# Kernel tuning notes

Hardware: AMD Instinct MI355X
Metric: run time of the kernel (lower is better)

Reference implementation:

```python
import jax, jax.numpy as jnp
import numpy as np

N, E, IN, H, T = 100000, 1600000, 10, 64, 10


def setup_inputs() -> dict:
    key = jax.random.key(0)
    ks = jax.random.split(key, 24)
    w = lambda k, shape, s=0.05: jax.random.normal(k, shape, jnp.float32) * s
    return {
        "x": w(ks[0], (N, IN), 1.0),
        "edge_attr": w(ks[1], (E, T), 1.0),
        "gcn1_w": w(ks[2], (IN, H)), "gcn1_b": jnp.zeros((H,), jnp.float32),
        "e_w1": w(ks[3], (3 * T, H)), "e_b1": jnp.zeros((H,), jnp.float32),
        "e_w2": w(ks[4], (H, H)), "e_b2": jnp.zeros((H,), jnp.float32),
        "gcn2_w": w(ks[5], (2 * H, H)), "gcn2_b": jnp.zeros((H,), jnp.float32),
        "gcn3_w": w(ks[6], (H, IN)), "gcn3_b": jnp.zeros((IN,), jnp.float32),
        "l1_w": w(ks[7], (2 * IN, IN)), "l1_b": jnp.zeros((IN,), jnp.float32),
        "l2_w": w(ks[8], (IN, 128)), "l2_b": jnp.zeros((128,), jnp.float32),
        "l3_w": w(ks[9], (128, 32)), "l3_b": jnp.zeros((32,), jnp.float32),
        "l4_w": w(ks[10], (32, 2)), "l4_b": jnp.zeros((2,), jnp.float32),
        "edge_index": jax.random.randint(ks[11], (2, E), 0, N),
    }


def reference(x, edge_attr, gcn1_w, gcn1_b, e_w1, e_b1, e_w2, e_b2,
              gcn2_w, gcn2_b, gcn3_w, gcn3_b, l1_w, l1_b, l2_w, l2_b,
              l3_w, l3_b, l4_w, l4_b, edge_index):
    src, dst = edge_index[0], edge_index[1]  # j -> i (message flows src->dst)
    # GCN symmetric norm with self loops: deg counted on target, +1 self loop
    deg = 1.0 + jax.ops.segment_sum(jnp.ones((E,), jnp.float32), dst, num_segments=N)
    dis = deg ** -0.5  # [N]
    edge_norm = (dis[src] * dis[dst])[:, None]  # [E,1]

    def gcn(h, w, b):
        hw = h @ w  # [N,out]
        agg = jax.ops.segment_sum(hw[src] * edge_norm, dst, num_segments=N)
        agg = agg + hw * (dis * dis)[:, None]  # self-loop term, norm = 1/deg
        return agg + b

    out1 = jax.nn.relu(gcn(x, gcn1_w, gcn1_b))
    # EdgeConv: gather x_i (dst), x_j (src), concat edge_attr, MLP, scatter-max
    m = jnp.concatenate([x[dst], x[src], edge_attr], axis=1)  # [E, 3T]
    m = jax.nn.relu(m @ e_w1 + e_b1) @ e_w2 + e_b2  # [E, H]
    agg = jax.ops.segment_max(m, dst, num_segments=N)
    agg = jnp.where(jnp.isfinite(agg), agg, 0.0)  # isolated nodes -> 0
    oute = jax.nn.relu(agg)

    out2 = jax.nn.relu(gcn(jnp.concatenate([out1, oute], axis=1), gcn2_w, gcn2_b))
    out3 = jax.nn.relu(gcn(out2, gcn3_w, gcn3_b))
    h = jnp.concatenate([x, out3], axis=1)  # [N, 2*IN]
    h = jax.nn.softplus(h @ l1_w + l1_b)
    h = jax.nn.softplus(h @ l2_w + l2_b)
    h = jax.nn.softplus(h @ l3_w + l3_b)
    h = h @ l4_w + l4_b  # [N, 2]
    return (h[:, 0], h[:, 1])
```

## Files before the change

### kernel.cpp

```cpp
#include <hip/hip_runtime.h>
#include <hip/hip_bf16.h>

typedef unsigned int u32;
typedef unsigned short u16;
typedef _Float16 f16;
typedef _Float16 f16x8 __attribute__((ext_vector_type(8)));
typedef float f32x4 __attribute__((ext_vector_type(4)));
typedef u32 u32x4 __attribute__((ext_vector_type(4)));

#define DEV static __device__ __forceinline__

#define O_G1   0
#define O_G1b  640
#define O_W1   704
#define O_B1   2624
#define O_W2   2688
#define O_B2   6784
#define O_G2   6848
#define O_G2b  15040
#define O_G3   15104
#define O_G3b  15744
#define O_L1   15754
#define O_L1b  15954
#define O_L2t  15964
#define O_L2b  17244
#define O_L3   17372
#define O_L3b  21468
#define O_L4t  21500
#define O_L4b  21564
#define O_WF1  21568
#define O_WF2  22592
#define WTOT   24640

#define ECNB   32

DEV float bfu(u16 h){ return __uint_as_float(((u32)h) << 16); }
DEV float bflo(u32 u){ return __uint_as_float(u << 16); }
DEV float bfhi(u32 u){ return __uint_as_float(u & 0xffff0000u); }
DEV u16 f2bf(float x){
  __hip_bfloat16 b = __float2bfloat16(x);
  return *(u16*)&b;
}
DEV float rdf(const void* p, int idx, int isf32){
  return isf32 ? ((const float*)p)[idx] : bfu(((const u16*)p)[idx]);
}
DEV void load10_bf(const u32* __restrict__ p, float* f){
  u32 a0=p[0],a1=p[1],a2=p[2],a3=p[3],a4=p[4];
  f[0]=bflo(a0); f[1]=bfhi(a0);
  f[2]=bflo(a1); f[3]=bfhi(a1);
  f[4]=bflo(a2); f[5]=bfhi(a2);
  f[6]=bflo(a3); f[7]=bfhi(a3);
  f[8]=bflo(a4); f[9]=bfhi(a4);
}
DEV void load10_any(const void* base, size_t row, int isf32, float* f){
  if (isf32){
    const float* p = (const float*)base + row*10;
    #pragma unroll
    for (int k=0;k<10;k++) f[k] = p[k];
  } else {
    load10_bf((const u32*)base + row*5, f);
  }
}
DEV float softplusf(float x){ return fmaxf(x,0.f) + log1pf(__expf(-fabsf(x))); }

DEV int permk(int k){
  if (k < 8)  return k;
  if (k < 16) return 10 + (k-8);
  if (k < 24) return 20 + (k-16);
  if (k == 24) return 8;
  if (k == 25) return 9;
  if (k == 26) return 18;
  if (k == 27) return 19;
  if (k == 28) return 28;
  if (k == 29) return 29;
  return -1;
}
DEV u32 packh2(float a, float b){
  union { f16 h[2]; u32 u; } t;
  t.h[0] = (f16)a; t.h[1] = (f16)b;
  return t.u;
}

__global__ __launch_bounds__(256) void k_detect(
    const u32* p0, const u32* p1, const u32* p2, const u32* p3,
    const u32* p4, const u32* p5, const u32* p6, const u32* p7,
    const u32* p8, const u32* p9, const u32* p10,const u32* p11,
    const u32* p12,const u32* p13,const u32* p14,const u32* p15,
    const u32* p16,const u32* p17,const u32* p18,const u32* p19,
    int* __restrict__ flags, int N_, int E_)
{
  int a = blockIdx.x;
  const u32* p;
  int elems;
  switch (a){
    case 0:  p=p0;  elems=N_*10; break;
    case 1:  p=p1;  elems=E_*10; break;
    case 2:  p=p2;  elems=640;  break;
    case 3:  p=p3;  elems=64;   break;
    case 4:  p=p4;  elems=1920; break;
    case 5:  p=p5;  elems=64;   break;
    case 6:  p=p6;  elems=4096; break;
    case 7:  p=p7;  elems=64;   break;
    case 8:  p=p8;  elems=8192; break;
    case 9:  p=p9;  elems=64;   break;
    case 10: p=p10; elems=640;  break;
    case 11: p=p11; elems=10;   break;
    case 12: p=p12; elems=200;  break;
    case 13: p=p13; elems=10;   break;
    case 14: p=p14; elems=1280; break;
    case 15: p=p15; elems=128;  break;
    case 16: p=p16; elems=4096; break;
    case 17: p=p17; elems=32;   break;
    case 18: p=p18; elems=64;   break;
    default: p=p19; elems=2;    break;
  }
  int nw = elems/2; if (nw > 512) nw = 512; if (nw < 1) nw = 1;
  int localA = 0, localZ = 0;
  for (int i=threadIdx.x; i<nw; i+=256){
    u32 w = p[i];
    u32 ex = (w >> 7) & 0xffu;
    if (ex >= 0x90u) localA++;
    if ((w & 0xffffu) == 0u) localZ++;
  }
  int packed = (localA << 16) | localZ;
  __shared__ int red[4];
  #pragma unroll
  for (int off=32; off; off>>=1) packed += __shfl_down(packed, off);
  if ((threadIdx.x & 63) == 0) red[threadIdx.x>>6] = packed;
  __syncthreads();
  if (threadIdx.x == 0){
    int s = red[0]+red[1]+red[2]+red[3];
    int sA = s >> 16, sZ = s & 0xffff;
    flags[a] = (sA * 16 >= nw || sZ * 4 >= nw * 3) ? 1 : 0;
  }
}

__global__ __launch_bounds__(256) void k_prep(
    const void* g1w, const void* g1b, const void* ew1, const void* eb1,
    const void* ew2, const void* eb2, const void* g2w, const void* g2b,
    const void* g3w, const void* g3b, const void* l1w, const void* l1b,
    const void* l2w, const void* l2b, const void* l3w, const void* l3b,
    const void* l4w, const void* l4b,
    const int* __restrict__ flags, float* __restrict__ W)
{
  int t = threadIdx.x;
  int f2=flags[2],f3=flags[3],f4=flags[4],f5=flags[5],f6=flags[6],f7=flags[7];
  int f8=flags[8],f9=flags[9],f10=flags[10],f11=flags[11],f12=flags[12],f13=flags[13];
  int f14=flags[14],f15=flags[15],f16=flags[16],f17=flags[17],f18=flags[18],f19=flags[19];
  for (int i=t;i<640;i+=256)  W[O_G1+i]  = rdf(g1w,i,f2);
  for (int i=t;i<64;i+=256)   W[O_G1b+i] = rdf(g1b,i,f3);
  for (int i=t;i<1920;i+=256) W[O_W1+i]  = rdf(ew1,i,f4);
  for (int i=t;i<64;i+=256)   W[O_B1+i]  = rdf(eb1,i,f5);
  for (int i=t;i<4096;i+=256) W[O_W2+i]  = rdf(ew2,i,f6);
  for (int i=t;i<64;i+=256)   W[O_B2+i]  = rdf(eb2,i,f7);
  for (int i=t;i<8192;i+=256) W[O_G2+i]  = rdf(g2w,i,f8);
  for (int i=t;i<64;i+=256)   W[O_G2b+i] = rdf(g2b,i,f9);
  for (int i=t;i<640;i+=256)  W[O_G3+i]  = rdf(g3w,i,f10);
  for (int i=t;i<10;i+=256)   W[O_G3b+i] = rdf(g3b,i,f11);
  for (int i=t;i<200;i+=256)  W[O_L1+i]  = rdf(l1w,i,f12);
  for (int i=t;i<10;i+=256)   W[O_L1b+i] = rdf(l1b,i,f13);
  for (int i=t;i<1280;i+=256){ int o=i/10,k=i-o*10; W[O_L2t+i]=rdf(l2w,k*128+o,f14); }
  for (int i=t;i<128;i+=256)  W[O_L2b+i] = rdf(l2b,i,f15);
  for (int i=t;i<4096;i+=256) W[O_L3+i]  = rdf(l3w,i,f16);
  for (int i=t;i<32;i+=256)   W[O_L3b+i] = rdf(l3b,i,f17);
  for (int i=t;i<64;i+=256){ int c=i>>5,j=i&31; W[O_L4t+i]=rdf(l4w,j*2+c,f18); }
  for (int i=t;i<2;i+=256)    W[O_L4b+i] = rdf(l4b,i,f19);
  u32* Wu = (u32*)W;
  for (int i=t;i<1024;i+=256){
    int l=i&63, q=(i>>6)&3, c=i>>8;
    int k0=(l>>4)*8+2*q, col=c*16+(l&15);
    int r0=permk(k0), r1=permk(k0+1);
    float v0 = (r0<0)?0.f:rdf(ew1,r0*64+col,f4);
    float v1 = (r1<0)?0.f:rdf(ew1,r1*64+col,f4);
    Wu[O_WF1+i] = packh2(v0,v1);
  }
  for (int i=t;i<2048;i+=256){
    int l=i&63, q=(i>>6)&3, h2=(i>>8)&1, c=i>>9;
    int k0=32*h2+(l>>4)*8+2*q, col=c*16+(l&15);
    Wu[O_WF2+i] = packh2(rdf(ew2,k0*64+col,f6), rdf(ew2,(k0+1)*64+col,f6));
  }
}

__global__ __launch_bounds__(256) void k_init(int* __restrict__ cnt, int N_)
{
  int i = blockIdx.x*256 + threadIdx.x;
  if (i < N_) cnt[i] = 0;
}

__global__ __launch_bounds__(256) void k_count(const int* __restrict__ ei, int* __restrict__ cnt, int E_)
{
  int e = blockIdx.x*256 + threadIdx.x;
  if (e >= E_) return;
  atomicAdd(&cnt[ei[E_+e]], 1);
}

__global__ __launch_bounds__(1024) void k_bsum(const int* __restrict__ cnt, int* __restrict__ bsum, int N_)
{
  int i = blockIdx.x*1024 + threadIdx.x;
  int v = (i < N_) ? cnt[i] : 0;
  #pragma unroll
  for (int off=32; off; off>>=1) v += __shfl_down(v, off);
  __shared__ int ws_[16];
  if ((threadIdx.x & 63) == 0) ws_[threadIdx.x>>6] = v;
  __syncthreads();
  if (threadIdx.x == 0){
    int s = 0;
    #pragma unroll
    for (int j=0;j<16;j++) s += ws_[j];
    bsum[blockIdx.x] = s;
  }
}

__global__ __launch_bounds__(128) void k_scan_small(const int* __restrict__ bsum, int* __restrict__ boff, int NB)
{
  int t = threadIdx.x;
  int v = (t < NB) ? bsum[t] : 0;
  int lane = t & 63, w = t >> 6;
  int x = v;
  #pragma unroll
  for (int off=1; off<64; off<<=1){ int y=__shfl_up(x,off); if (lane>=off) x+=y; }
  __shared__ int t2[2];
  if (lane==63) t2[w]=x;
  __syncthreads();
  if (w==1) x += t2[0];
  boff[t] = x - v;
}

__global__ __launch_bounds__(1024) void k_scan_final(
    int* __restrict__ cnt, const int* __restrict__ boff,
    int* __restrict__ rp, float* __restrict__ dis, int N_, int E_)
{
  int i = blockIdx.x*1024 + threadIdx.x;
  int v = (i < N_) ? cnt[i] : 0;
  int lane = threadIdx.x & 63, w = threadIdx.x >> 6;
  int x = v;
  #pragma unroll
  for (int off=1; off<64; off<<=1){ int y=__shfl_up(x,off); if (lane>=off) x+=y; }
  __shared__ int wp[16];
  if (lane==63) wp[w]=x;
  __syncthreads();
  if (threadIdx.x==0){
    int run=0;
    #pragma unroll
    for (int j=0;j<16;j++){ int t=wp[j]; wp[j]=run; run+=t; }
  }
  __syncthreads();
  int incl = x + wp[w] + boff[blockIdx.x];
  if (i < N_){
    rp[i]  = incl - v;
    dis[i] = rsqrtf(1.f + (float)v);
    cnt[i] = 0;
  }
  if (i == 0) rp[N_] = E_;
}

__global__ __launch_bounds__(256) void k_fill(
    const int* __restrict__ ei, const int* __restrict__ rp, int* __restrict__ cnt,
    int4* __restrict__ csr, int E_)
{
  int e = blockIdx.x*256 + threadIdx.x;
  if (e >= E_) return;
  int s = ei[e], d = ei[E_+e];
  int pos = rp[d] + atomicAdd(&cnt[d], 1);
  csr[pos] = make_int4(s, e, d, 0);
}

#define EC_EMIT \
  if (run >= 0){ int bb = run*64 + x; \
    atomicMax(&nodemax[bb],    __float_as_int(e0)); \
    atomicMax(&nodemax[bb+16], __float_as_int(e1)); \
    atomicMax(&nodemax[bb+32], __float_as_int(e2)); \
    atomicMax(&nodemax[bb+48], __float_as_int(e3)); }
#define EC_STEP(DD, RR) { \
  float t0=fmaxf(mcv[0][RR],0.f), t1=fmaxf(mcv[1][RR],0.f), \
        t2=fmaxf(mcv[2][RR],0.f), t3=fmaxf(mcv[3][RR],0.f); \
  if (DD == run){ e0=fmaxf(e0,t0); e1=fmaxf(e1,t1); e2=fmaxf(e2,t2); e3=fmaxf(e3,t3); } \
  else { EC_EMIT; run = DD; e0=t0; e1=t1; e2=t2; e3=t3; } }

__global__ __launch_bounds__(256) void k_edgeconv(
    const void* __restrict__ xv, const void* __restrict__ eav,
    const int* __restrict__ rp, const int4* __restrict__ csr,
    const float* __restrict__ W, const int* __restrict__ flags,
    float* __restrict__ oute, int N_, int E_)
{
  __shared__ int nodemax[ECNB*64];
  __shared__ u32 hbuf[4][16*36];
  int tid = threadIdx.x;
  int l = tid & 63, wv = tid >> 6;
  int x = l & 15, g = l >> 4;
  int n0 = blockIdx.x * ECNB;
  if (n0 >= N_) return;
  int nend = n0 + ECNB; if (nend > N_) nend = N_;
  #pragma unroll
  for (int i=0;i<ECNB/4;i++) nodemax[i*256 + tid] = 0;
  int fx = flags[0], fea = flags[1];
  const u32* Wu = (const u32*)W;
  union FU { u32 u[4]; f16x8 v; };
  union HU { f16 h[8]; u32 u[4]; f16x8 v; };
  FU w1u[4];
  #pragma unroll
  for (int c=0;c<4;c++){
    #pragma unroll
    for (int q=0;q<4;q++) w1u[c].u[q] = Wu[O_WF1 + (c*4+q)*64 + l];
  }
  FU w2u[4][2];
  #pragma unroll
  for (int c=0;c<4;c++){
    #pragma unroll
    for (int h=0;h<2;h++){
      #pragma unroll
      for (int q=0;q<4;q++) w2u[c][h].u[q] = Wu[O_WF2 + ((c*2+h)*4+q)*64 + l];
    }
  }
  float b1v[4], b2v[4];
  #pragma unroll
  for (int c=0;c<4;c++){ b1v[c] = (W+O_B1)[c*16 + x]; b2v[c] = (W+O_B2)[c*16 + x]; }
  int pbase = rp[n0], pend = rp[nend];
  int ntiles = (pend - pbase + 15) >> 4;
  u32* hb = hbuf[wv];
  __syncthreads();

  for (int t = wv; t < ntiles; t += 4){
    int p0 = pbase + t*16;
    int eA = p0 + x; if (eA > E_-1) eA = E_-1;
    int4 ce = csr[eA];
    HU af;
    u32 exv = 0;
    if (g < 3){
      long row; const void* base; int isf;
      if (g==0){ row = ce.z; base = xv;  isf = fx; }
      else if (g==1){ row = ce.x; base = xv;  isf = fx; }
      else { row = ce.y; base = eav; isf = fea; }
      if (isf){
        const float* p = (const float*)base + row*10;
        #pragma unroll
        for (int j=0;j<8;j++) af.h[j] = (f16)p[j];
        exv = packh2(p[8], p[9]);
      } else {
        const u32* p = (const u32*)base + row*5;
        u32 a0=p[0],a1=p[1],a2=p[2],a3=p[3],a4=p[4];
        af.h[0]=(f16)bflo(a0); af.h[1]=(f16)bfhi(a0);
        af.h[2]=(f16)bflo(a1); af.h[3]=(f16)bfhi(a1);
        af.h[4]=(f16)bflo(a2); af.h[5]=(f16)bfhi(a2);
        af.h[6]=(f16)bflo(a3); af.h[7]=(f16)bfhi(a3);
        exv = packh2(bflo(a4), bfhi(a4));
      }
    }
    u32 ge0 = (u32)__shfl((int)exv, x);
    u32 ge1 = (u32)__shfl((int)exv, x+16);
    u32 ge2 = (u32)__shfl((int)exv, x+32);
    if (g == 3){ af.u[0]=ge0; af.u[1]=ge1; af.u[2]=ge2; af.u[3]=0; }
    int pe = p0 + 4*g;
    int dz = ce.z;
    int d0 = __shfl(dz, 4*g+0); d0 = (pe   < pend) ? d0 - n0 : -1;
    int d1 = __shfl(dz, 4*g+1); d1 = (pe+1 < pend) ? d1 - n0 : -1;
    int d2 = __shfl(dz, 4*g+2); d2 = (pe+2 < pend) ? d2 - n0 : -1;
    int d3 = __shfl(dz, 4*g+3); d3 = (pe+3 < pend) ? d3 - n0 : -1;
    f32x4 z = {0.f,0.f,0.f,0.f};
    f32x4 hc[4];
    #pragma unroll
    for (int c=0;c<4;c++)
      hc[c] = __builtin_amdgcn_mfma_f32_16x16x32_f16(af.v, w1u[c].v, z, 0, 0, 0);
    #pragma unroll
    for (int r=0;r<4;r++){
      u32 pk0,pk1,pk2,pk3;
      {
        float hv = fmaxf(hc[0][r] + b1v[0], 0.f);
        union { f16 h; u16 u; } cv; cv.h=(f16)hv; u32 mine=cv.u;
        u32 other=(u32)__shfl_xor((int)mine,1,64);
        pk0 = (x&1) ? (other|(mine<<16)) : (mine|(other<<16));
      }{
        float hv = fmaxf(hc[1][r] + b1v[1], 0.f);
        union { f16 h; u16 u; } cv; cv.h=(f16)hv; u32 mine=cv.u;
        u32 other=(u32)__shfl_xor((int)mine,1,64);
        pk1 = (x&1) ? (other|(mine<<16)) : (mine|(other<<16));
      }{
        float hv = fmaxf(hc[2][r] + b1v[2], 0.f);
        union { f16 h; u16 u; } cv; cv.h=(f16)hv; u32 mine=cv.u;
        u32 other=(u32)__shfl_xor((int)mine,1,64);
        pk2 = (x&1) ? (other|(mine<<16)) : (mine|(other<<16));
      }{
        float hv = fmaxf(hc[3][r] + b1v[3], 0.f);
        union { f16 h; u16 u; } cv; cv.h=(f16)hv; u32 mine=cv.u;
        u32 other=(u32)__shfl_xor((int)mine,1,64);
        pk3 = (x&1) ? (other|(mine<<16)) : (mine|(other<<16));
      }
      int edge = 4*g + r;
      int par = (x&1) ? 16 : 0;
      hb[edge*36 + par + (x>>1)]     = (x&1) ? pk2 : pk0;
      hb[edge*36 + 8 + par + (x>>1)] = (x&1) ? pk3 : pk1;
    }
    asm volatile("s_waitcnt lgkmcnt(0)" ::: "memory");
    HU a2f[2];
    #pragma unroll
    for (int h=0;h<2;h++){
      const u32x4* p = (const u32x4*)&hb[x*36 + g*4 + 16*h];
      u32x4 tv = *p;
      a2f[h].u[0]=tv[0]; a2f[h].u[1]=tv[1]; a2f[h].u[2]=tv[2]; a2f[h].u[3]=tv[3];
    }
    f32x4 mcv[4];
    #pragma unroll
    for (int c=0;c<4;c++){
      f32x4 bi = {b2v[c],b2v[c],b2v[c],b2v[c]};
      f32x4 acc = __builtin_amdgcn_mfma_f32_16x16x32_f16(a2f[0].v, w2u[c][0].v, bi, 0, 0, 0);
      mcv[c]    = __builtin_amdgcn_mfma_f32_16x16x32_f16(a2f[1].v, w2u[c][1].v, acc, 0, 0, 0);
    }
    int run = -2; float e0=0.f,e1=0.f,e2=0.f,e3=0.f;
    EC_STEP(d0,0) EC_STEP(d1,1) EC_STEP(d2,2) EC_STEP(d3,3)
    EC_EMIT;
  }
  __syncthreads();
  int tot = (nend - n0) * 64;
  for (int i = tid; i < tot; i += 256)
    oute[(size_t)n0*64 + i] = __int_as_float(nodemax[i]);
}

__global__ __launch_bounds__(256) void k_aggx(
    const void* __restrict__ xv, const int* __restrict__ rp,
    const int4* __restrict__ csr, const float* __restrict__ dis,
    const int* __restrict__ flags, float* __restrict__ sx, int N_)
{
  int i = blockIdx.x*256 + threadIdx.x;
  if (i >= N_) return;
  int fx = flags[0];
  float di = dis[i], d2 = di*di;
  float acc[10], ac2[10], tA[10], tB[10], tC[10], tD[10];
  load10_any(xv, (size_t)i, fx, tA);
  #pragma unroll
  for (int f=0;f<10;f++){ acc[f] = tA[f]*d2; ac2[f] = 0.f; }
  int b = rp[i], en = rp[i+1];
  int p = b;
  for (; p+3 < en; p += 4){
    int s0 = csr[p].x, s1 = csr[p+1].x, s2 = csr[p+2].x, s3 = csr[p+3].x;
    float m0 = dis[s0]*di, m1 = dis[s1]*di, m2 = dis[s2]*di, m3 = dis[s3]*di;
    load10_any(xv, (size_t)s0, fx, tA);
    load10_any(xv, (size_t)s1, fx, tB);
    load10_any(xv, (size_t)s2, fx, tC);
    load10_any(xv, (size_t)s3, fx, tD);
    #pragma unroll
    for (int f=0;f<10;f++){
      acc[f] = fmaf(tA[f], m0, acc[f]);
      ac2[f] = fmaf(tB[f], m1, ac2[f]);
      acc[f] = fmaf(tC[f], m2, acc[f]);
      ac2[f] = fmaf(tD[f], m3, ac2[f]);
    }
  }
  for (; p < en; p++){
    int s0 = csr[p].x; float m0 = dis[s0]*di;
    load10_any(xv, (size_t)s0, fx, tA);
    #pragma unroll
    for (int f=0;f<10;f++) acc[f] = fmaf(tA[f], m0, acc[f]);
  }
  float* o = sx + (size_t)i*10;
  #pragma unroll
  for (int f=0;f<10;f++) o[f] = acc[f] + ac2[f];
}

__global__ __launch_bounds__(256) void k_hw2(
    const float* __restrict__ sx, const float* __restrict__ oute,
    const float* __restrict__ W, u16* __restrict__ hw2o, int N_)
{
  int i = blockIdx.x*256 + threadIdx.x;
  if (i >= N_) return;
  float sv[10];
  const float* srow = sx + (size_t)i*10;
  #pragma unroll
  for (int f=0;f<10;f++) sv[f] = srow[f];
  const float* __restrict__ G1  = W + O_G1;
  const float* __restrict__ G1b = W + O_G1b;
  const float* __restrict__ G2  = W + O_G2;
  float hw[64];
  #pragma unroll
  for (int f=0;f<64;f++) hw[f] = 0.f;
  #pragma unroll 1
  for (int k=0;k<64;k++){
    float o1 = G1b[k];
    #pragma unroll
    for (int j=0;j<10;j++) o1 = fmaf(sv[j], G1[j*64+k], o1);
    o1 = fmaxf(o1, 0.f);
    const float* __restrict__ wt = G2 + k*64;
    #pragma unroll
    for (int f=0;f<64;f++) hw[f] = fmaf(o1, wt[f], hw[f]);
  }
  const float* orow = oute + (size_t)i*64;
  #pragma unroll 1
  for (int k=0;k<64;k++){
    float ov = orow[k];
    const float* __restrict__ wb = G2 + (64+k)*64;
    #pragma unroll
    for (int f=0;f<64;f++) hw[f] = fmaf(ov, wb[f], hw[f]);
  }
  u16* out = hw2o + (size_t)i*64;
  #pragma unroll
  for (int f=0;f<64;f++) out[f] = f2bf(hw[f]);
}

__global__ __launch_bounds__(256) void k_agg64(
    const u16* __restrict__ hw2, const int* __restrict__ rp,
    const int4* __restrict__ csr, const float* __restrict__ dis,
    const float* __restrict__ W, float* __restrict__ out2, int N_)
{
  int i = (blockIdx.x*256 + threadIdx.x) >> 6;
  int lane = threadIdx.x & 63;
  if (i >= N_) return;
  int e4 = lane >> 4, c4 = lane & 15;
  float di = dis[i];
  int b = rp[i], en = rp[i+1];
  const uint2* __restrict__ h2 = (const uint2*)hw2;
  float a0=0.f,a1=0.f,a2=0.f,a3=0.f;
  float b0=0.f,b1=0.f,b2=0.f,b3=0.f;
  int p = b + e4;
  int sA = (p   < en) ? csr[p].x   : 0;
  int sB = (p+4 < en) ? csr[p+4].x : 0;
  for (; p + 4 < en; p += 8){
    int sAn = (p+8  < en) ? csr[p+8].x  : 0;
    int sBn = (p+12 < en) ? csr[p+12].x : 0;
    float nmA = dis[sA]*di, nmB = dis[sB]*di;
    uint2 wA = h2[(size_t)sA*16 + c4];
    uint2 wB = h2[(size_t)sB*16 + c4];
    a0 = fmaf(bflo(wA.x), nmA, a0); a1 = fmaf(bfhi(wA.x), nmA, a1);
    a2 = fmaf(bflo(wA.y), nmA, a2); a3 = fmaf(bfhi(wA.y), nmA, a3);
    b0 = fmaf(bflo(wB.x), nmB, b0); b1 = fmaf(bfhi(wB.x), nmB, b1);
    b2 = fmaf(bflo(wB.y), nmB, b2); b3 = fmaf(bfhi(wB.y), nmB, b3);
    sA = sAn; sB = sBn;
  }
  if (p < en){
    float nmA = dis[sA]*di;
    uint2 wA = h2[(size_t)sA*16 + c4];
    a0 = fmaf(bflo(wA.x), nmA, a0); a1 = fmaf(bfhi(wA.x), nmA, a1);
    a2 = fmaf(bflo(wA.y), nmA, a2); a3 = fmaf(bfhi(wA.y), nmA, a3);
  }
  a0 += b0; a1 += b1; a2 += b2; a3 += b3;
  a0 += __shfl_xor(a0,16); a1 += __shfl_xor(a1,16);
  a2 += __shfl_xor(a2,16); a3 += __shfl_xor(a3,16);
  a0 += __shfl_xor(a0,32); a1 += __shfl_xor(a1,32);
  a2 += __shfl_xor(a2,32); a3 += __shfl_xor(a3,32);
  if (e4 == 0){
    uint2 ws2 = h2[(size_t)i*16 + c4];
    float d2 = di*di;
    const float* G2b = W + O_G2b;
    float4 o;
    o.x = fmaxf(fmaf(bflo(ws2.x), d2, a0) + G2b[4*c4],   0.f);
    o.y = fmaxf(fmaf(bfhi(ws2.x), d2, a1) + G2b[4*c4+1], 0.f);
    o.z = fmaxf(fmaf(bflo(ws2.y), d2, a2) + G2b[4*c4+2], 0.f);
    o.w = fmaxf(fmaf(bfhi(ws2.y), d2, a3) + G2b[4*c4+3], 0.f);
    *(float4*)(out2 + (size_t)i*64 + 4*c4) = o;
  }
}

__global__ __launch_bounds__(256) void k_hw3(
    const float* __restrict__ out2, const float* __restrict__ W,
    float* __restrict__ hw3, int N_)
{
  int i = blockIdx.x*256 + threadIdx.x;
  if (i >= N_) return;
  const float* row = out2 + (size_t)i*64;
  const float* __restrict__ G3 = W + O_G3;
  float a[10];
  #pragma unroll
  for (int f=0;f<10;f++) a[f] = 0.f;
  #pragma unroll 1
  for (int k=0;k<64;k++){
    float v = row[k];
    const float* __restrict__ w = G3 + k*10;
    #pragma unroll
    for (int f=0;f<10;f++) a[f] = fmaf(v, w[f], a[f]);
  }
  float* o = hw3 + (size_t)i*10;
  #pragma unroll
  for (int f=0;f<10;f++) o[f] = a[f];
}

__global__ __launch_bounds__(256) void k_final(
    const void* __restrict__ xv, const float* __restrict__ hw3,
    const int* __restrict__ rp, const int4* __restrict__ csr,
    const float* __restrict__ dis, const int* __restrict__ flags,
    const float* __restrict__ W, float* __restrict__ out, int N_)
{
  int i = blockIdx.x*256 + threadIdx.x;
  if (i >= N_) return;
  int fx = flags[0];
  float di = dis[i];
  float a[10], a2v[10];
  const float* hrow = hw3 + (size_t)i*10;
  #pragma unroll
  for (int f=0;f<10;f++){ a[f] = hrow[f]*di*di; a2v[f] = 0.f; }
  int b = rp[i], en = rp[i+1];
  int p = b;
  for (; p+3 < en; p += 4){
    int s0 = csr[p].x, s1 = csr[p+1].x, s2 = csr[p+2].x, s3 = csr[p+3].x;
    float m0 = dis[s0]*di, m1 = dis[s1]*di, m2 = dis[s2]*di, m3 = dis[s3]*di;
    const float* r0p = hw3 + (size_t)s0*10;
    const float* r1p = hw3 + (size_t)s1*10;
    const float* r2p = hw3 + (size_t)s2*10;
    const float* r3p = hw3 + (size_t)s3*10;
    #pragma unroll
    for (int f=0;f<10;f++){
      a[f]   = fmaf(r0p[f], m0, a[f]);
      a2v[f] = fmaf(r1p[f], m1, a2v[f]);
      a[f]   = fmaf(r2p[f], m2, a[f]);
      a2v[f] = fmaf(r3p[f], m3, a2v[f]);
    }
  }
  for (; p < en; p++){
    int s0 = csr[p].x; float m0 = dis[s0]*di;
    const float* r0p = hw3 + (size_t)s0*10;
    #pragma unroll
    for (int f=0;f<10;f++) a[f] = fmaf(r0p[f], m0, a[f]);
  }
  #pragma unroll
  for (int f=0;f<10;f++) a[f] += a2v[f];
  const float* G3b = W + O_G3b;
  float h20[20];
  load10_any(xv, (size_t)i, fx, h20);
  #pragma unroll
  for (int f=0;f<10;f++) h20[10+f] = fmaxf(a[f] + G3b[f], 0.f);
  const float* __restrict__ L1  = W + O_L1;
  const float* __restrict__ L1b = W + O_L1b;
  float h1[10];
  #pragma unroll
  for (int f=0;f<10;f++) h1[f] = L1b[f];
  #pragma unroll
  for (int k=0;k<20;k++){
    float v = h20[k];
    const float* __restrict__ w = L1 + k*10;
    #pragma unroll
    for (int f=0;f<10;f++) h1[f] = fmaf(v, w[f], h1[f]);
  }
  #pragma unroll
  for (int f=0;f<10;f++) h1[f] = softplusf(h1[f]);
  const float* __restrict__ L2t = W + O_L2t;
  const float* __restrict__ L2b = W + O_L2b;
  const float* __restrict__ L3  = W + O_L3;
  const float* __restrict__ L3b = W + O_L3b;
  float h3a[32];
  #pragma unroll
  for (int j=0;j<32;j++) h3a[j] = L3b[j];
  #pragma unroll 1
  for (int o=0;o<128;o++){
    float s2 = L2b[o];
    const float* __restrict__ wt = L2t + o*10;
    #pragma unroll
    for (int k=0;k<10;k++) s2 = fmaf(h1[k], wt[k], s2);
    s2 = softplusf(s2);
    const float* __restrict__ w3 = L3 + o*32;
    #pragma unroll
    for (int j=0;j<32;j++) h3a[j] = fmaf(s2, w3[j], h3a[j]);
  }
  const float* L4t = W + O_L4t;
  const float* L4b = W + O_L4b;
  float r0 = L4b[0], r1 = L4b[1];
  #pragma unroll
  for (int j=0;j<32;j++){
    float h3 = softplusf(h3a[j]);
    r0 = fmaf(h3, L4t[j],    r0);
    r1 = fmaf(h3, L4t[32+j], r1);
  }
  out[i]      = r0;
  out[N_ + i] = r1;
}

extern "C" void kernel_launch(void* const* d_in, const int* in_sizes, int n_in,
                              void* d_out, int out_size, void* d_ws, size_t ws_size,
                              hipStream_t stream)
{
  const void* xv  = d_in[0];
  const void* eav = d_in[1];
  const int*  ei  = (const int*)d_in[20];
  int N_ = in_sizes[0] / 10;
  int E_ = in_sizes[1] / 10;

  float* W = (float*)d_ws;
  size_t off = WTOT;
  int*   cnt   = (int*)(W + off);   off += (size_t)N_;
  int*   rp    = (int*)(W + off);   off += (size_t)N_ + 1;
  float* dis   = (float*)(W + off); off += (size_t)N_;
  int*   bsum  = (int*)(W + off);   off += 256;
  int*   boff  = (int*)(W + off);   off += 256;
  int*   flags = (int*)(W + off);   off += 32;
  off = (off + 3) & ~(size_t)3;
  int4*  csr   = (int4*)(W + off);  off += (size_t)E_ * 4;
  float* oute  = (float*)(W + off);
  float* out2  = oute;
  off += (size_t)N_ * 64;
  u16*   hw2   = (u16*)(W + off);   off += (size_t)N_ * 32;
  float* sx    = (float*)(W + off);
  float* hw3   = sx;
  off += (size_t)N_ * 10;

  if (ws_size < off * sizeof(float)) return;

  int gN = (N_ + 255)/256, gE = (E_ + 255)/256;
  int NB = (N_ + 1023)/1024;

  k_detect<<<20,256,0,stream>>>(
      (const u32*)d_in[0],(const u32*)d_in[1],
      (const u32*)d_in[2],(const u32*)d_in[3],(const u32*)d_in[4],(const u32*)d_in[5],
      (const u32*)d_in[6],(const u32*)d_in[7],(const u32*)d_in[8],(const u32*)d_in[9],
      (const u32*)d_in[10],(const u32*)d_in[11],(const u32*)d_in[12],(const u32*)d_in[13],
      (const u32*)d_in[14],(const u32*)d_in[15],(const u32*)d_in[16],(const u32*)d_in[17],
      (const u32*)d_in[18],(const u32*)d_in[19],
      flags, N_, E_);
  k_prep<<<1,256,0,stream>>>(
      d_in[2],d_in[3],d_in[4],d_in[5],d_in[6],d_in[7],d_in[8],d_in[9],
      d_in[10],d_in[11],d_in[12],d_in[13],d_in[14],d_in[15],d_in[16],d_in[17],
      d_in[18],d_in[19], flags, W);
  k_init<<<gN,256,0,stream>>>(cnt, N_);
  k_count<<<gE,256,0,stream>>>(ei, cnt, E_);
  k_bsum<<<NB,1024,0,stream>>>(cnt, bsum, N_);
  k_scan_small<<<1,128,0,stream>>>(bsum, boff, NB);
  k_scan_final<<<NB,1024,0,stream>>>(cnt, boff, rp, dis, N_, E_);
  k_fill<<<gE,256,0,stream>>>(ei, rp, cnt, csr, E_);
  k_edgeconv<<<(N_+ECNB-1)/ECNB,256,0,stream>>>(xv, eav, rp, csr, W, flags, oute, N_, E_);
  k_aggx<<<gN,256,0,stream>>>(xv, rp, csr, dis, flags, sx, N_);
  k_hw2<<<gN,256,0,stream>>>(sx, oute, W, hw2, N_);
  k_agg64<<<(N_+3)/4,256,0,stream>>>(hw2, rp, csr, dis, W, out2, N_);
  k_hw3<<<gN,256,0,stream>>>(out2, W, hw3, N_);
  k_final<<<gN,256,0,stream>>>(xv, hw3, rp, csr, dis, flags, W,
                               (float*)d_out, N_);
}
```

Measured before the change: 730.1 us.

## Split per-node work across four lanes in aggx, hw2, hw3 and final kernels

Four node-level kernels now give each node four lanes instead of one thread. The aggregation kernels interleave each node's edges across the lanes and combine partial sums with xor shuffles. The dense kernels split output columns or reduction terms across the lanes. The aim is more parallelism and memory-level parallelism on a 100k-node graph (about 400 blocks before), along with fewer registers per thread. In exchange it adds shuffle reductions, divergence on small-degree nodes, and redundant loads of shared row data.

```diff
diff --git a/kernel.cpp b/kernel.cpp
--- a/kernel.cpp
+++ b/kernel.cpp
@@ -420,47 +420,58 @@
     const int4* __restrict__ csr, const float* __restrict__ dis,
     const int* __restrict__ flags, float* __restrict__ sx, int N_)
 {
-  int i = blockIdx.x*256 + threadIdx.x;
+  int t = blockIdx.x*256 + threadIdx.x;
+  int i = t >> 2, q = t & 3;
   if (i >= N_) return;
   int fx = flags[0];
   float di = dis[i], d2 = di*di;
-  float acc[10], ac2[10], tA[10], tB[10], tC[10], tD[10];
-  load10_any(xv, (size_t)i, fx, tA);
-  #pragma unroll
-  for (int f=0;f<10;f++){ acc[f] = tA[f]*d2; ac2[f] = 0.f; }
+  float acc[10], ac2[10], tA[10], tB[10];
+  #pragma unroll
+  for (int f=0;f<10;f++){ acc[f] = 0.f; ac2[f] = 0.f; }
+  if (q == 0){
+    load10_any(xv, (size_t)i, fx, tA);
+    #pragma unroll
+    for (int f=0;f<10;f++) acc[f] = tA[f]*d2;
+  }
   int b = rp[i], en = rp[i+1];
-  int p = b;
-  for (; p+3 < en; p += 4){
-    int s0 = csr[p].x, s1 = csr[p+1].x, s2 = csr[p+2].x, s3 = csr[p+3].x;
-    float m0 = dis[s0]*di, m1 = dis[s1]*di, m2 = dis[s2]*di, m3 = dis[s3]*di;
+  int p = b + q;
+  for (; p+4 < en; p += 8){
+    int s0 = csr[p].x, s1 = csr[p+4].x;
+    float m0 = dis[s0]*di, m1 = dis[s1]*di;
     load10_any(xv, (size_t)s0, fx, tA);
     load10_any(xv, (size_t)s1, fx, tB);
-    load10_any(xv, (size_t)s2, fx, tC);
-    load10_any(xv, (size_t)s3, fx, tD);
     #pragma unroll
     for (int f=0;f<10;f++){
       acc[f] = fmaf(tA[f], m0, acc[f]);
       ac2[f] = fmaf(tB[f], m1, ac2[f]);
-      acc[f] = fmaf(tC[f], m2, acc[f]);
-      ac2[f] = fmaf(tD[f], m3, ac2[f]);
     }
   }
-  for (; p < en; p++){
+  if (p < en){
     int s0 = csr[p].x; float m0 = dis[s0]*di;
     load10_any(xv, (size_t)s0, fx, tA);
     #pragma unroll
     for (int f=0;f<10;f++) acc[f] = fmaf(tA[f], m0, acc[f]);
   }
-  float* o = sx + (size_t)i*10;
-  #pragma unroll
-  for (int f=0;f<10;f++) o[f] = acc[f] + ac2[f];
+  #pragma unroll
+  for (int f=0;f<10;f++){
+    float v = acc[f] + ac2[f];
+    v += __shfl_xor(v, 1);
+    v += __shfl_xor(v, 2);
+    acc[f] = v;
+  }
+  if (q == 0){
+    float* o = sx + (size_t)i*10;
+    #pragma unroll
+    for (int f=0;f<10;f++) o[f] = acc[f];
+  }
 }
 
 __global__ __launch_bounds__(256) void k_hw2(
     const float* __restrict__ sx, const float* __restrict__ oute,
     const float* __restrict__ W, u16* __restrict__ hw2o, int N_)
 {
-  int i = blockIdx.x*256 + threadIdx.x;
+  int t = blockIdx.x*256 + threadIdx.x;
+  int i = t >> 2, q = t & 3;
   if (i >= N_) return;
   float sv[10];
   const float* srow = sx + (size_t)i*10;
@@ -468,10 +479,10 @@
   for (int f=0;f<10;f++) sv[f] = srow[f];
   const float* __restrict__ G1  = W + O_G1;
   const float* __restrict__ G1b = W + O_G1b;
-  const float* __restrict__ G2  = W + O_G2;
-  float hw[64];
-  #pragma unroll
-  for (int f=0;f<64;f++) hw[f] = 0.f;
+  const float* __restrict__ G2  = W + O_G2 + q*16;
+  float hw[16];
+  #pragma unroll
+  for (int f=0;f<16;f++) hw[f] = 0.f;
   #pragma unroll 1
   for (int k=0;k<64;k++){
     float o1 = G1b[k];
@@ -480,7 +491,7 @@
     o1 = fmaxf(o1, 0.f);
     const float* __restrict__ wt = G2 + k*64;
     #pragma unroll
-    for (int f=0;f<64;f++) hw[f] = fmaf(o1, wt[f], hw[f]);
+    for (int f=0;f<16;f++) hw[f] = fmaf(o1, wt[f], hw[f]);
   }
   const float* orow = oute + (size_t)i*64;
   #pragma unroll 1
@@ -488,11 +499,12 @@
     float ov = orow[k];
     const float* __restrict__ wb = G2 + (64+k)*64;
     #pragma unroll
-    for (int f=0;f<64;f++) hw[f] = fmaf(ov, wb[f], hw[f]);
-  }
-  u16* out = hw2o + (size_t)i*64;
-  #pragma unroll
-  for (int f=0;f<64;f++) out[f] = f2bf(hw[f]);
+    for (int f=0;f<16;f++) hw[f] = fmaf(ov, wb[f], hw[f]);
+  }
+  u32* out = (u32*)(hw2o + (size_t)i*64) + q*8;
+  #pragma unroll
+  for (int f=0;f<16;f+=2)
+    out[f>>1] = (u32)f2bf(hw[f]) | ((u32)f2bf(hw[f+1]) << 16);
 }
 
 __global__ __launch_bounds__(256) void k_agg64(
@@ -552,7 +564,8 @@
     const float* __restrict__ out2, const float* __restrict__ W,
     float* __restrict__ hw3, int N_)
 {
-  int i = blockIdx.x*256 + threadIdx.x;
+  int t = blockIdx.x*256 + threadIdx.x;
+  int i = t >> 2, q = t & 3;
   if (i >= N_) return;
   const float* row = out2 + (size_t)i*64;
   const float* __restrict__ G3 = W + O_G3;
@@ -560,15 +573,24 @@
   #pragma unroll
   for (int f=0;f<10;f++) a[f] = 0.f;
   #pragma unroll 1
-  for (int k=0;k<64;k++){
+  for (int k=q; k<64; k+=4){
     float v = row[k];
     const float* __restrict__ w = G3 + k*10;
     #pragma unroll
     for (int f=0;f<10;f++) a[f] = fmaf(v, w[f], a[f]);
   }
-  float* o = hw3 + (size_t)i*10;
-  #pragma unroll
-  for (int f=0;f<10;f++) o[f] = a[f];
+  #pragma unroll
+  for (int f=0;f<10;f++){
+    float v = a[f];
+    v += __shfl_xor(v, 1);
+    v += __shfl_xor(v, 2);
+    a[f] = v;
+  }
+  if (q == 0){
+    float* o = hw3 + (size_t)i*10;
+    #pragma unroll
+    for (int f=0;f<10;f++) o[f] = a[f];
+  }
 }
 
 __global__ __launch_bounds__(256) void k_final(
@@ -577,39 +599,46 @@
     const float* __restrict__ dis, const int* __restrict__ flags,
     const float* __restrict__ W, float* __restrict__ out, int N_)
 {
-  int i = blockIdx.x*256 + threadIdx.x;
+  int t = blockIdx.x*256 + threadIdx.x;
+  int i = t >> 2, q = t & 3;
   if (i >= N_) return;
   int fx = flags[0];
   float di = dis[i];
   float a[10], a2v[10];
-  const float* hrow = hw3 + (size_t)i*10;
-  #pragma unroll
-  for (int f=0;f<10;f++){ a[f] = hrow[f]*di*di; a2v[f] = 0.f; }
+  #pragma unroll
+  for (int f=0;f<10;f++){ a[f] = 0.f; a2v[f] = 0.f; }
+  if (q == 0){
+    const float* hrow = hw3 + (size_t)i*10;
+    float d2 = di*di;
+    #pragma unroll
+    for (int f=0;f<10;f++) a[f] = hrow[f]*d2;
+  }
   int b = rp[i], en = rp[i+1];
-  int p = b;
-  for (; p+3 < en; p += 4){
-    int s0 = csr[p].x, s1 = csr[p+1].x, s2 = csr[p+2].x, s3 = csr[p+3].x;
-    float m0 = dis[s0]*di, m1 = dis[s1]*di, m2 = dis[s2]*di, m3 = dis[s3]*di;
+  int p = b + q;
+  for (; p+4 < en; p += 8){
+    int s0 = csr[p].x, s1 = csr[p+4].x;
+    float m0 = dis[s0]*di, m1 = dis[s1]*di;
     const float* r0p = hw3 + (size_t)s0*10;
     const float* r1p = hw3 + (size_t)s1*10;
-    const float* r2p = hw3 + (size_t)s2*10;
-    const float* r3p = hw3 + (size_t)s3*10;
     #pragma unroll
     for (int f=0;f<10;f++){
       a[f]   = fmaf(r0p[f], m0, a[f]);
       a2v[f] = fmaf(r1p[f], m1, a2v[f]);
-      a[f]   = fmaf(r2p[f], m2, a[f]);
-      a2v[f] = fmaf(r3p[f], m3, a2v[f]);
     }
   }
-  for (; p < en; p++){
+  if (p < en){
     int s0 = csr[p].x; float m0 = dis[s0]*di;
     const float* r0p = hw3 + (size_t)s0*10;
     #pragma unroll
     for (int f=0;f<10;f++) a[f] = fmaf(r0p[f], m0, a[f]);
   }
   #pragma unroll
-  for (int f=0;f<10;f++) a[f] += a2v[f];
+  for (int f=0;f<10;f++){
+    float v = a[f] + a2v[f];
+    v += __shfl_xor(v, 1);
+    v += __shfl_xor(v, 2);
+    a[f] = v;
+  }
   const float* G3b = W + O_G3b;
   float h20[20];
   load10_any(xv, (size_t)i, fx, h20);
@@ -635,9 +664,9 @@
   const float* __restrict__ L3b = W + O_L3b;
   float h3a[32];
   #pragma unroll
-  for (int j=0;j<32;j++) h3a[j] = L3b[j];
+  for (int j=0;j<32;j++) h3a[j] = (q == 0) ? L3b[j] : 0.f;
   #pragma unroll 1
-  for (int o=0;o<128;o++){
+  for (int o=q; o<128; o+=4){
     float s2 = L2b[o];
     const float* __restrict__ wt = L2t + o*10;
     #pragma unroll
@@ -647,17 +676,29 @@
     #pragma unroll
     for (int j=0;j<32;j++) h3a[j] = fmaf(s2, w3[j], h3a[j]);
   }
+  #pragma unroll
+  for (int j=0;j<32;j++){
+    float v = h3a[j];
+    v += __shfl_xor(v, 1);
+    v += __shfl_xor(v, 2);
+    h3a[j] = v;
+  }
   const float* L4t = W + O_L4t;
   const float* L4b = W + O_L4b;
-  float r0 = L4b[0], r1 = L4b[1];
-  #pragma unroll
-  for (int j=0;j<32;j++){
+  float r0 = 0.f, r1 = 0.f;
+  #pragma unroll
+  for (int u=0; u<8; u++){
+    int j = q*8 + u;
     float h3 = softplusf(h3a[j]);
     r0 = fmaf(h3, L4t[j],    r0);
     r1 = fmaf(h3, L4t[32+j], r1);
   }
-  out[i]      = r0;
-  out[N_ + i] = r1;
+  r0 += __shfl_xor(r0,1); r0 += __shfl_xor(r0,2);
+  r1 += __shfl_xor(r1,1); r1 += __shfl_xor(r1,2);
+  if (q == 0){
+    out[i]      = r0 + L4b[0];
+    out[N_ + i] = r1 + L4b[1];
+  }
 }
 
 extern "C" void kernel_launch(void* const* d_in, const int* in_sizes, int n_in,
@@ -691,6 +732,7 @@
   if (ws_size < off * sizeof(float)) return;
 
   int gN = (N_ + 255)/256, gE = (E_ + 255)/256;
+  int gQ = (N_ + 63)/64;
   int NB = (N_ + 1023)/1024;
 
   k_detect<<<20,256,0,stream>>>(
@@ -712,10 +754,10 @@
   k_scan_final<<<NB,1024,0,stream>>>(cnt, boff, rp, dis, N_, E_);
   k_fill<<<gE,256,0,stream>>>(ei, rp, cnt, csr, E_);
   k_edgeconv<<<(N_+ECNB-1)/ECNB,256,0,stream>>>(xv, eav, rp, csr, W, flags, oute, N_, E_);
-  k_aggx<<<gN,256,0,stream>>>(xv, rp, csr, dis, flags, sx, N_);
-  k_hw2<<<gN,256,0,stream>>>(sx, oute, W, hw2, N_);
+  k_aggx<<<gQ,256,0,stream>>>(xv, rp, csr, dis, flags, sx, N_);
+  k_hw2<<<gQ,256,0,stream>>>(sx, oute, W, hw2, N_);
   k_agg64<<<(N_+3)/4,256,0,stream>>>(hw2, rp, csr, dis, W, out2, N_);
-  k_hw3<<<gN,256,0,stream>>>(out2, W, hw3, N_);
-  k_final<<<gN,256,0,stream>>>(xv, hw3, rp, csr, dis, flags, W,
+  k_hw3<<<gQ,256,0,stream>>>(out2, W, hw3, N_);
+  k_final<<<gQ,256,0,stream>>>(xv, hw3, rp, csr, dis, flags, W,
                                (float*)d_out, N_);
 }
```

Measured after the change: 1.007 ms. 37.9% more time.
